# Performance work log

Measured on AMD Instinct MI355X. Metric: run time of the kernel, lower is better.

Reference implementation:

```python
import jax, jax.numpy as jnp
import numpy as np

B, T, C, HS = 8, 4096, 1024, 64
HALF = HS // 2
ROPE_BASE = 10000.0


def _rope_tables(t_len, half_dim, base=ROPE_BASE):
    inv_freq = base ** (-jnp.arange(half_dim, dtype=jnp.float32) / half_dim)
    freqs = jnp.arange(t_len, dtype=jnp.float32)[:, None] * inv_freq[None, :]  # (T, D/2)
    return jnp.cos(freqs), jnp.sin(freqs)


def apply_rope(x, cos, sin):
    # x: (B, T, D) with interleaved even/odd pairs; cos/sin: (T, D/2)
    x_even = x[..., ::2]
    x_odd = x[..., 1::2]
    r_even = x_even * cos[None] - x_odd * sin[None]
    r_odd = x_even * sin[None] + x_odd * cos[None]
    # re-interleave
    return jnp.stack([r_even, r_odd], axis=-1).reshape(x.shape)


def setup_inputs() -> dict:
    key = jax.random.key(0)
    kx, kq, kk, kv = jax.random.split(key, 4)
    s = 1.0 / np.sqrt(C)
    cos, sin = _rope_tables(T, HALF)
    return {
        "x": jax.random.normal(kx, (B, T, C), dtype=jnp.float32),
        "cos": cos,
        "sin": sin,
        "Wq": jax.random.normal(kq, (C, HS), dtype=jnp.float32) * s,
        "Wk": jax.random.normal(kk, (C, HS), dtype=jnp.float32) * s,
        "Wv": jax.random.normal(kv, (C, HS), dtype=jnp.float32) * s,
    }


def reference(x, cos, sin, Wq, Wk, Wv):
    # q/k/v projections (bias-free Linear)
    q = jnp.einsum('btc,cd->btd', x, Wq)
    k = jnp.einsum('btc,cd->btd', x, Wk)
    v = jnp.einsum('btc,cd->btd', x, Wv)
    q = apply_rope(q, cos, sin)
    k = apply_rope(k, cos, sin)
    t = x.shape[1]
    scale = 1.0 / jnp.sqrt(jnp.asarray(k.shape[-1], dtype=x.dtype))
    wei = jnp.einsum('bqd,bkd->bqk', q, k) * scale  # (B, T, T)
    causal = jnp.tril(jnp.ones((t, t), dtype=bool))
    wei = jnp.where(causal[None], wei, -jnp.inf)
    wei = jax.nn.softmax(wei, axis=-1)
    # dropout = 0.0 (eval mode)
    return jnp.einsum('bqk,bkd->bqd', wei, v)
```

## Files before the change

### kernel.cpp

```cpp
#include <hip/hip_runtime.h>
#include <hip/hip_bf16.h>

#define BB 8
#define TT 4096
#define CC 1024
#define HS 64

typedef __attribute__((ext_vector_type(8))) __bf16 bf16x8;
typedef __attribute__((ext_vector_type(4))) __bf16 bf16x4;
typedef __attribute__((ext_vector_type(4))) float f32x4;

static __device__ __forceinline__ unsigned pack_bf16(float a, float b) {
    unsigned short ua = __builtin_bit_cast(unsigned short, (__bf16)a);
    unsigned short ub = __builtin_bit_cast(unsigned short, (__bf16)b);
    return (unsigned)ua | ((unsigned)ub << 16);
}

__global__ __launch_bounds__(256) void wprep_kernel(
    const float* __restrict__ Wq, const float* __restrict__ Wk,
    const float* __restrict__ Wv, __bf16* __restrict__ Wt)
{
    int i = blockIdx.x * 256 + threadIdx.x;
    int dr = i >> 10;
    int c  = i & 1023;
    int m  = dr >> 6;
    int d  = dr & 63;
    const float* src = (m == 0) ? Wq : ((m == 1) ? Wk : Wv);
    float v = src[(long)c * HS + d];
    if (m == 0) v *= 0.125f * 1.4426950408889634f;
    Wt[i] = (__bf16)v;
}

__global__ __launch_bounds__(256) void qkv_rope_kernel(
    const float* __restrict__ x,
    const float* __restrict__ cosT,
    const float* __restrict__ sinT,
    const __bf16* __restrict__ Wt,
    __bf16* __restrict__ Qo, __bf16* __restrict__ Ko, __bf16* __restrict__ Vo)
{
    __shared__ __bf16 xs[64][72];
    __shared__ __bf16 Wl[192][72];

    const int tid  = threadIdx.x;
    const int lane = tid & 63;
    const int w    = tid >> 6;
    const int col  = lane & 15;
    const int grp  = lane >> 4;
    const long rowbase = (long)blockIdx.x * 64;

    f32x4 acc[12];
#pragma unroll
    for (int i = 0; i < 12; i++) acc[i] = 0.0f;

    for (int ck = 0; ck < CC; ck += 64) {
        {
            int r = tid >> 2, c0 = (tid & 3) * 16;
            const float4* src = (const float4*)(x + (rowbase + r) * (long)CC + ck + c0);
#pragma unroll
            for (int i = 0; i < 4; i++) {
                float4 v = src[i];
                bf16x4 t;
                t[0] = (__bf16)v.x; t[1] = (__bf16)v.y;
                t[2] = (__bf16)v.z; t[3] = (__bf16)v.w;
                *(bf16x4*)&xs[r][c0 + i * 4] = t;
            }
        }
        {
#pragma unroll
            for (int i = 0; i < 6; i++) {
                int u = i * 256 + tid;
                int dr = u >> 3, cu = (u & 7) * 8;
                bf16x8 v = *(const bf16x8*)(Wt + (long)dr * CC + ck + cu);
                *(bf16x8*)&Wl[dr][cu] = v;
            }
        }
        __syncthreads();
#pragma unroll
        for (int s = 0; s < 2; s++) {
            bf16x8 a = *(const bf16x8*)&xs[w * 16 + col][s * 32 + grp * 8];
#pragma unroll
            for (int nf = 0; nf < 12; nf++) {
                bf16x8 b = *(const bf16x8*)&Wl[nf * 16 + col][s * 32 + grp * 8];
                acc[nf] = __builtin_amdgcn_mfma_f32_16x16x32_bf16(a, b, acc[nf], 0, 0, 0);
            }
        }
        __syncthreads();
    }

#pragma unroll
    for (int r = 0; r < 4; r++) {
        long grow = rowbase + w * 16 + grp * 4 + r;
        int t = (int)(grow & (TT - 1));
        const float* cp = cosT + (long)t * 32;
        const float* sp = sinT + (long)t * 32;
#pragma unroll
        for (int nf = 0; nf < 4; nf++) {
            int ii = nf * 8 + (col >> 1);
            float cs = cp[ii], sn = sp[ii];
            float sgn_sn = (col & 1) ? sn : -sn;
            float qv = acc[nf][r];
            float qp = __shfl_xor(qv, 1);
            float qo = qv * cs + qp * sgn_sn;
            float kv = acc[nf + 4][r];
            float kp = __shfl_xor(kv, 1);
            float ko = kv * cs + kp * sgn_sn;
            long base = grow * HS + nf * 16 + col;
            Qo[base] = (__bf16)qo;
            Ko[base] = (__bf16)ko;
            xs[nf * 16 + col][w * 16 + grp * 4 + r] = (__bf16)acc[nf + 8][r];
        }
    }
    __syncthreads();
    {
        int d = tid >> 2, seg = tid & 3;
        int b  = (int)(rowbase >> 12);
        int t0 = (int)(rowbase & (TT - 1));
        bf16x8 v0 = *(const bf16x8*)&xs[d][seg * 16];
        bf16x8 v1 = *(const bf16x8*)&xs[d][seg * 16 + 8];
        __bf16* dst = Vo + ((size_t)b * 64 + d) * TT + t0 + seg * 16;
        *(bf16x8*)dst = v0;
        *(bf16x8*)(dst + 8) = v1;
    }
}

__global__ __launch_bounds__(256, 3) void attn_kernel(
    const __bf16* __restrict__ Q, const __bf16* __restrict__ K,
    const __bf16* __restrict__ Vt, float* __restrict__ O,
    float* __restrict__ Opart, float* __restrict__ mlbuf)
{
    __shared__ __bf16 Kl[2][64 * 64];
    __shared__ __bf16 Vl[2][64 * 64];
    __shared__ __align__(16) unsigned char plds[4][2048];

    const int tid  = threadIdx.x;
    const int lane = tid & 63;
    const int col  = lane & 15;
    const int g    = lane >> 4;
    const int w    = tid >> 6;

    const int n   = blockIdx.x;
    const int b   = n & 7;
    const int idx = n >> 3;
    int qt, j0, j1, ch;
    bool partial;
    if (idx < 32)      { qt = 32 + idx;  j0 = 0;  j1 = 32;     partial = true;  ch = 0; }
    else if (idx < 64) { qt = idx;       j0 = 32; j1 = qt + 1; partial = true;  ch = 1; }
    else               { qt = 95 - idx;  j0 = 0;  j1 = qt + 1; partial = false; ch = 0; }

    const int qloc = qt * 64 + w * 16 + col;
    const size_t qrow = (size_t)b * TT + qloc;
    bf16x8 qb[2];
#pragma unroll
    for (int s = 0; s < 2; s++)
        qb[s] = *(const bf16x8*)(Q + qrow * HS + s * 32 + g * 8);

    const int r0 = tid >> 3, c0 = tid & 7;
    const int r1 = r0 + 32;
    const __bf16* Kbase = K + (size_t)b * TT * HS;
    const __bf16* Vbase = Vt + (size_t)b * 64 * TT;

#define SWZ(row, cb) (((row) << 6) | (((cb) ^ ((row) & 7)) << 3))

    f32x4 acc[4];
#pragma unroll
    for (int i = 0; i < 4; i++) acc[i] = 0.f;
    float mrun = -3e38f;
    float lsum0 = 0.f, lsum1 = 0.f, lsum2 = 0.f, lsum3 = 0.f;

    unsigned char* pbase = plds[w] + col * 128;
    const int sw = col & 7;

    bf16x8 sk0, sk1, sv0, sv1;
    auto stageLoad = [&](int j) {
        const __bf16* kp = Kbase + (size_t)(j * 64) * HS;
        sk0 = *(const bf16x8*)(kp + r0 * HS + c0 * 8);
        sk1 = *(const bf16x8*)(kp + r1 * HS + c0 * 8);
        const __bf16* vp = Vbase + j * 64;
        sv0 = *(const bf16x8*)(vp + (size_t)r0 * TT + c0 * 8);
        sv1 = *(const bf16x8*)(vp + (size_t)r1 * TT + c0 * 8);
    };
    auto stageWrite = [&](int buf) {
        *(bf16x8*)&Kl[buf][SWZ(r0, c0)] = sk0;
        *(bf16x8*)&Kl[buf][SWZ(r1, c0)] = sk1;
        *(bf16x8*)&Vl[buf][SWZ(r0, c0)] = sv0;
        *(bf16x8*)&Vl[buf][SWZ(r1, c0)] = sv1;
    };

    stageLoad(j0);
    stageWrite(0);
    __syncthreads();

    int cur = 0;
    for (int j = j0; j < j1; ++j) {
        const bool more = (j + 1 < j1);
        if (more) {
            stageLoad(j + 1);
        }
        __builtin_amdgcn_sched_barrier(0);

        f32x4 sf[4];
#pragma unroll
        for (int i = 0; i < 4; i++) sf[i] = 0.f;
        {
            bf16x8 kf[8];
#pragma unroll
            for (int nf = 0; nf < 4; nf++)
#pragma unroll
                for (int s = 0; s < 2; s++)
                    kf[nf * 2 + s] = *(const bf16x8*)&Kl[cur][SWZ(nf * 16 + col, s * 4 + g)];
            __builtin_amdgcn_s_setprio(1);
#pragma unroll
            for (int s = 0; s < 2; s++)
#pragma unroll
                for (int nf = 0; nf < 4; nf++)
                    sf[nf] = __builtin_amdgcn_mfma_f32_16x16x32_bf16(kf[nf * 2 + s], qb[s], sf[nf], 0, 0, 0);
            __builtin_amdgcn_s_setprio(0);
        }
        if (j == qt) {
#pragma unroll
            for (int nf = 0; nf < 4; nf++)
#pragma unroll
                for (int r = 0; r < 4; r++)
                    if (j * 64 + nf * 16 + g * 4 + r > qloc) sf[nf][r] = -3e38f;
        }
        float fm[4];
#pragma unroll
        for (int f = 0; f < 4; f++)
            fm[f] = fmaxf(fmaxf(sf[f][0], sf[f][1]), fmaxf(sf[f][2], sf[f][3]));
        float mt = fmaxf(fmaxf(fm[0], fm[1]), fmaxf(fm[2], fm[3]));
        if (!__all(mt <= mrun + 8.0f)) {
            float mg = fmaxf(mt, __shfl_xor(mt, 16));
            mg = fmaxf(mg, __shfl_xor(mg, 32));
            float mn = fmaxf(mrun, mg);
            float al = exp2f(mrun - mn);
            mrun = mn;
            lsum0 *= al; lsum1 *= al; lsum2 *= al; lsum3 *= al;
#pragma unroll
            for (int nf = 0; nf < 4; nf++) acc[nf] *= al;
        }
#pragma unroll
        for (int f = 0; f < 4; f++) {
            float p0 = exp2f(sf[f][0] - mrun);
            float p1 = exp2f(sf[f][1] - mrun);
            float p2 = exp2f(sf[f][2] - mrun);
            float p3 = exp2f(sf[f][3] - mrun);
            sf[f][0] = p0; sf[f][1] = p1; sf[f][2] = p2; sf[f][3] = p3;
            lsum0 += p0; lsum1 += p1; lsum2 += p2; lsum3 += p3;
        }
#pragma unroll
        for (int nf = 0; nf < 4; nf++) {
            uint2 val;
            val.x = pack_bf16(sf[nf][0], sf[nf][1]);
            val.y = pack_bf16(sf[nf][2], sf[nf][3]);
            *(uint2*)(pbase + ((((nf * 2 + (g >> 1)) ^ sw) << 4) | ((g & 1) << 3))) = val;
        }
        {
            bf16x8 vf[8];
#pragma unroll
            for (int nf = 0; nf < 4; nf++)
#pragma unroll
                for (int s = 0; s < 2; s++)
                    vf[nf * 2 + s] = *(const bf16x8*)&Vl[cur][SWZ(nf * 16 + col, s * 4 + g)];
            __builtin_amdgcn_s_setprio(1);
#pragma unroll
            for (int s = 0; s < 2; s++) {
                bf16x8 pf = *(const bf16x8*)(pbase + (((s * 4 + g) ^ sw) << 4));
#pragma unroll
                for (int nf = 0; nf < 4; nf++)
                    acc[nf] = __builtin_amdgcn_mfma_f32_16x16x32_bf16(vf[nf * 2 + s], pf, acc[nf], 0, 0, 0);
            }
            __builtin_amdgcn_s_setprio(0);
        }
        if (more) {
            stageWrite(cur ^ 1);
        }
        __syncthreads();
        cur ^= 1;
    }

    float ls = (lsum0 + lsum1) + (lsum2 + lsum3);
    ls += __shfl_xor(ls, 16);
    ls += __shfl_xor(ls, 32);

    if (!partial) {
        float rinv = __builtin_amdgcn_rcpf(ls);
        float* orow = O + qrow * HS;
#pragma unroll
        for (int nf = 0; nf < 4; nf++) {
            float4 v;
            v.x = acc[nf][0] * rinv; v.y = acc[nf][1] * rinv;
            v.z = acc[nf][2] * rinv; v.w = acc[nf][3] * rinv;
            *(float4*)(orow + nf * 16 + g * 4) = v;
        }
    } else {
        const int slot = (b * 32 + (qt - 32)) * 2 + ch;
        float* prow = Opart + ((size_t)slot * 64 + w * 16 + col) * 64;
#pragma unroll
        for (int nf = 0; nf < 4; nf++) {
            float4 v;
            v.x = acc[nf][0]; v.y = acc[nf][1];
            v.z = acc[nf][2]; v.w = acc[nf][3];
            *(float4*)(prow + nf * 16 + g * 4) = v;
        }
        if (g == 0) {
            float2 mv = make_float2(mrun, ls);
            *(float2*)(mlbuf + ((size_t)slot * 64 + w * 16 + col) * 2) = mv;
        }
    }
#undef SWZ
}

__global__ __launch_bounds__(256) void combine_kernel(
    const float* __restrict__ Opart, const float* __restrict__ mlbuf,
    float* __restrict__ O)
{
    const int qi = blockIdx.x;
    const int b  = blockIdx.y;
    const int row = threadIdx.x >> 2;
    const int seg = threadIdx.x & 3;
    const int slot0 = (b * 32 + qi) * 2;

    const float* p0 = mlbuf + ((size_t)slot0 * 64 + row) * 2;
    const float* p1 = mlbuf + ((size_t)(slot0 + 1) * 64 + row) * 2;
    float m0 = p0[0], l0 = p0[1];
    float m1 = p1[0], l1 = p1[1];
    float M  = fmaxf(m0, m1);
    float w0 = exp2f(m0 - M), w1 = exp2f(m1 - M);
    float rinv = 1.0f / (l0 * w0 + l1 * w1);
    w0 *= rinv; w1 *= rinv;

    const float4* s0 = (const float4*)(Opart + ((size_t)slot0 * 64 + row) * 64 + seg * 16);
    const float4* s1 = (const float4*)(Opart + ((size_t)(slot0 + 1) * 64 + row) * 64 + seg * 16);
    float4* dst = (float4*)(O + ((size_t)b * TT + (32 + qi) * 64 + row) * 64 + seg * 16);
#pragma unroll
    for (int i = 0; i < 4; i++) {
        float4 a = s0[i], c = s1[i];
        float4 v;
        v.x = a.x * w0 + c.x * w1;
        v.y = a.y * w0 + c.y * w1;
        v.z = a.z * w0 + c.z * w1;
        v.w = a.w * w0 + c.w * w1;
        dst[i] = v;
    }
}

extern "C" void kernel_launch(void* const* d_in, const int* in_sizes, int n_in,
                              void* d_out, int out_size, void* d_ws, size_t ws_size,
                              hipStream_t stream)
{
    const float* x    = (const float*)d_in[0];
    const float* cosT = (const float*)d_in[1];
    const float* sinT = (const float*)d_in[2];
    const float* Wq   = (const float*)d_in[3];
    const float* Wk   = (const float*)d_in[4];
    const float* Wv   = (const float*)d_in[5];
    float* out = (float*)d_out;

    __bf16* Qb = (__bf16*)d_ws;
    __bf16* Kb = Qb + (size_t)BB * TT * HS;
    __bf16* Vb = Kb + (size_t)BB * TT * HS;
    __bf16* Wt = Vb + (size_t)BB * TT * HS;

    const size_t base_bytes = (size_t)3 * BB * TT * HS * 2 + 192 * 1024 * 2;
    float* Opart = (float*)((char*)d_ws + ((base_bytes + 255) & ~(size_t)255));
    float* mlbuf = Opart + (size_t)8 * 32 * 2 * 64 * 64;

    wprep_kernel<<<(192 * 1024) / 256, 256, 0, stream>>>(Wq, Wk, Wv, Wt);
    qkv_rope_kernel<<<(BB * TT) / 64, 256, 0, stream>>>(x, cosT, sinT, Wt, Qb, Kb, Vb);
    attn_kernel<<<768, 256, 0, stream>>>(Qb, Kb, Vb, out, Opart, mlbuf);
    combine_kernel<<<dim3(32, 8), 256, 0, stream>>>(Opart, mlbuf, out);
}
```

Measured before the change: 89.69 us.

## Software-pipeline QK^T of next tile with softmax/PV of previous tile

Restructures the attention inner loop so each iteration computes QK^T for tile j while doing the softmax and PV MFMA for tile j-1. V staging goes to a triple buffer and two score register sets alternate, so the MFMA work can overlap the exp/max VALU work. This costs more registers (an extra score fragment), which may pressure the 3-waves-per-SIMD occupancy target, and adds 8KB of LDS.

```diff
diff --git a/kernel.cpp b/kernel.cpp
--- a/kernel.cpp
+++ b/kernel.cpp
@@ -129,7 +129,7 @@
     float* __restrict__ Opart, float* __restrict__ mlbuf)
 {
     __shared__ __bf16 Kl[2][64 * 64];
-    __shared__ __bf16 Vl[2][64 * 64];
+    __shared__ __bf16 Vl[3][64 * 64];
     __shared__ __align__(16) unsigned char plds[4][2048];
 
     const int tid  = threadIdx.x;
@@ -179,54 +179,51 @@
         sv0 = *(const bf16x8*)(vp + (size_t)r0 * TT + c0 * 8);
         sv1 = *(const bf16x8*)(vp + (size_t)r1 * TT + c0 * 8);
     };
-    auto stageWrite = [&](int buf) {
-        *(bf16x8*)&Kl[buf][SWZ(r0, c0)] = sk0;
-        *(bf16x8*)&Kl[buf][SWZ(r1, c0)] = sk1;
-        *(bf16x8*)&Vl[buf][SWZ(r0, c0)] = sv0;
-        *(bf16x8*)&Vl[buf][SWZ(r1, c0)] = sv1;
-    };
-
-    stageLoad(j0);
-    stageWrite(0);
-    __syncthreads();
-
-    int cur = 0;
-    for (int j = j0; j < j1; ++j) {
-        const bool more = (j + 1 < j1);
-        if (more) {
-            stageLoad(j + 1);
-        }
-        __builtin_amdgcn_sched_barrier(0);
-
-        f32x4 sf[4];
-#pragma unroll
-        for (int i = 0; i < 4; i++) sf[i] = 0.f;
-        {
-            bf16x8 kf[8];
+    auto stageWriteK = [&](int kb) {
+        *(bf16x8*)&Kl[kb][SWZ(r0, c0)] = sk0;
+        *(bf16x8*)&Kl[kb][SWZ(r1, c0)] = sk1;
+    };
+    auto stageWriteV = [&](int vb) {
+        *(bf16x8*)&Vl[vb][SWZ(r0, c0)] = sv0;
+        *(bf16x8*)&Vl[vb][SWZ(r1, c0)] = sv1;
+    };
+
+    f32x4 sfA[4], sfB[4];
+
+    auto qkPhase = [&](int jv, f32x4 (&SF)[4]) {
+        bf16x8 kf[8];
+#pragma unroll
+        for (int nf = 0; nf < 4; nf++)
+#pragma unroll
+            for (int s = 0; s < 2; s++)
+                kf[nf * 2 + s] = *(const bf16x8*)&Kl[jv & 1][SWZ(nf * 16 + col, s * 4 + g)];
+        __builtin_amdgcn_s_setprio(1);
+#pragma unroll
+        for (int s = 0; s < 2; s++)
 #pragma unroll
             for (int nf = 0; nf < 4; nf++)
-#pragma unroll
-                for (int s = 0; s < 2; s++)
-                    kf[nf * 2 + s] = *(const bf16x8*)&Kl[cur][SWZ(nf * 16 + col, s * 4 + g)];
-            __builtin_amdgcn_s_setprio(1);
+                SF[nf] = __builtin_amdgcn_mfma_f32_16x16x32_bf16(kf[nf * 2 + s], qb[s], SF[nf], 0, 0, 0);
+        __builtin_amdgcn_s_setprio(0);
+    };
+
+    auto finPhase = [&](int jv, f32x4 (&SF)[4], int vb) {
+        bf16x8 vf[8];
+#pragma unroll
+        for (int nf = 0; nf < 4; nf++)
 #pragma unroll
             for (int s = 0; s < 2; s++)
-#pragma unroll
-                for (int nf = 0; nf < 4; nf++)
-                    sf[nf] = __builtin_amdgcn_mfma_f32_16x16x32_bf16(kf[nf * 2 + s], qb[s], sf[nf], 0, 0, 0);
-            __builtin_amdgcn_s_setprio(0);
-        }
-        if (j == qt) {
+                vf[nf * 2 + s] = *(const bf16x8*)&Vl[vb][SWZ(nf * 16 + col, s * 4 + g)];
+        if (jv == qt) {
 #pragma unroll
             for (int nf = 0; nf < 4; nf++)
 #pragma unroll
                 for (int r = 0; r < 4; r++)
-                    if (j * 64 + nf * 16 + g * 4 + r > qloc) sf[nf][r] = -3e38f;
+                    if (jv * 64 + nf * 16 + g * 4 + r > qloc) SF[nf][r] = -3e38f;
         }
         float fm[4];
 #pragma unroll
         for (int f = 0; f < 4; f++)
-            fm[f] = fmaxf(fmaxf(sf[f][0], sf[f][1]), fmaxf(sf[f][2], sf[f][3]));
+            fm[f] = fmaxf(fmaxf(SF[f][0], SF[f][1]), fmaxf(SF[f][2], SF[f][3]));
         float mt = fmaxf(fmaxf(fm[0], fm[1]), fmaxf(fm[2], fm[3]));
         if (!__all(mt <= mrun + 8.0f)) {
             float mg = fmaxf(mt, __shfl_xor(mt, 16));
@@ -240,43 +237,83 @@
         }
 #pragma unroll
         for (int f = 0; f < 4; f++) {
-            float p0 = exp2f(sf[f][0] - mrun);
-            float p1 = exp2f(sf[f][1] - mrun);
-            float p2 = exp2f(sf[f][2] - mrun);
-            float p3 = exp2f(sf[f][3] - mrun);
-            sf[f][0] = p0; sf[f][1] = p1; sf[f][2] = p2; sf[f][3] = p3;
+            float p0 = exp2f(SF[f][0] - mrun);
+            float p1 = exp2f(SF[f][1] - mrun);
+            float p2 = exp2f(SF[f][2] - mrun);
+            float p3 = exp2f(SF[f][3] - mrun);
+            SF[f][0] = p0; SF[f][1] = p1; SF[f][2] = p2; SF[f][3] = p3;
             lsum0 += p0; lsum1 += p1; lsum2 += p2; lsum3 += p3;
         }
 #pragma unroll
         for (int nf = 0; nf < 4; nf++) {
             uint2 val;
-            val.x = pack_bf16(sf[nf][0], sf[nf][1]);
-            val.y = pack_bf16(sf[nf][2], sf[nf][3]);
+            val.x = pack_bf16(SF[nf][0], SF[nf][1]);
+            val.y = pack_bf16(SF[nf][2], SF[nf][3]);
             *(uint2*)(pbase + ((((nf * 2 + (g >> 1)) ^ sw) << 4) | ((g & 1) << 3))) = val;
         }
-        {
-            bf16x8 vf[8];
+        __builtin_amdgcn_s_setprio(1);
+#pragma unroll
+        for (int s = 0; s < 2; s++) {
+            bf16x8 pf = *(const bf16x8*)(pbase + (((s * 4 + g) ^ sw) << 4));
 #pragma unroll
             for (int nf = 0; nf < 4; nf++)
-#pragma unroll
-                for (int s = 0; s < 2; s++)
-                    vf[nf * 2 + s] = *(const bf16x8*)&Vl[cur][SWZ(nf * 16 + col, s * 4 + g)];
-            __builtin_amdgcn_s_setprio(1);
-#pragma unroll
-            for (int s = 0; s < 2; s++) {
-                bf16x8 pf = *(const bf16x8*)(pbase + (((s * 4 + g) ^ sw) << 4));
-#pragma unroll
-                for (int nf = 0; nf < 4; nf++)
-                    acc[nf] = __builtin_amdgcn_mfma_f32_16x16x32_bf16(vf[nf * 2 + s], pf, acc[nf], 0, 0, 0);
-            }
-            __builtin_amdgcn_s_setprio(0);
-        }
+                acc[nf] = __builtin_amdgcn_mfma_f32_16x16x32_bf16(vf[nf * 2 + s], pf, acc[nf], 0, 0, 0);
+        }
+        __builtin_amdgcn_s_setprio(0);
+    };
+
+    auto iterStep = [&](int jv, f32x4 (&SFq)[4], f32x4 (&SFf)[4], int vb_f) {
+        const bool more = (jv + 1 < j1);
+        if (more) stageLoad(jv + 1);
+        __builtin_amdgcn_sched_barrier(0);
+#pragma unroll
+        for (int i = 0; i < 4; i++) SFq[i] = 0.f;
+        qkPhase(jv, SFq);
+        finPhase(jv - 1, SFf, vb_f);
         if (more) {
-            stageWrite(cur ^ 1);
+            stageWriteK((jv + 1) & 1);
+            stageWriteV(vb_f + 2 >= 3 ? vb_f - 1 : vb_f + 2);
         }
         __syncthreads();
-        cur ^= 1;
-    }
+    };
+
+    stageLoad(j0);
+    stageWriteK(j0 & 1);
+    const int vb0 = j0 % 3;
+    stageWriteV(vb0);
+    __syncthreads();
+
+    {
+        const bool more = (j0 + 1 < j1);
+        if (more) stageLoad(j0 + 1);
+        __builtin_amdgcn_sched_barrier(0);
+#pragma unroll
+        for (int i = 0; i < 4; i++) sfA[i] = 0.f;
+        qkPhase(j0, sfA);
+        if (more) {
+            stageWriteK((j0 + 1) & 1);
+            stageWriteV(vb0 + 1 >= 3 ? vb0 - 2 : vb0 + 1);
+        }
+        __syncthreads();
+    }
+
+    int vb_f = vb0;
+    int jv = j0 + 1;
+    while (jv + 1 < j1) {
+        iterStep(jv, sfB, sfA, vb_f);
+        vb_f = (vb_f + 1 >= 3) ? vb_f - 2 : vb_f + 1;
+        iterStep(jv + 1, sfA, sfB, vb_f);
+        vb_f = (vb_f + 1 >= 3) ? vb_f - 2 : vb_f + 1;
+        jv += 2;
+    }
+    bool lastIsB = false;
+    if (jv < j1) {
+        iterStep(jv, sfB, sfA, vb_f);
+        vb_f = (vb_f + 1 >= 3) ? vb_f - 2 : vb_f + 1;
+        lastIsB = true;
+    }
+    if (lastIsB) finPhase(j1 - 1, sfB, vb_f);
+    else         finPhase(j1 - 1, sfA, vb_f);
 
     float ls = (lsum0 + lsum1) + (lsum2 + lsum3);
     ls += __shfl_xor(ls, 16);
```

New measurement: 84.16 us. 6.2% less time.
